# Kernel optimization log

Measured on AMD Instinct MI355X. Metric: run time of the kernel, lower is better.

The kernel has to match this reference:

```python
import jax, jax.numpy as jnp
import numpy as np

# Hexagonal 7-tap kernel mask on a 3x3 grid (axial coords): corners (0,2) and (2,0) unused.
_HEX = np.ones((3, 3), np.float32)
_HEX[0, 2] = 0.0
_HEX[2, 0] = 0.0
HEX_MASK = jnp.asarray(_HEX)
BN_EPS = 1e-5


def ico_pad(x):
    # x: [B,C,H,W] with H = 5 charts stacked. Cross-chart wrap pad along H
    # (neighbor-chart gather), zero pad along W (corner_mode='zeros').
    x = jnp.pad(x, ((0, 0), (0, 0), (1, 1), (0, 0)), mode='wrap')
    x = jnp.pad(x, ((0, 0), (0, 0), (0, 0), (1, 1)))
    return x


def ico_conv(x, w):
    # hex conv = masked 3x3 conv on icosahedrally padded charts
    return jax.lax.conv_general_dilated(
        ico_pad(x), w * HEX_MASK, window_strides=(1, 1), padding='VALID',
        dimension_numbers=('NCHW', 'OIHW', 'NCHW'))


def ico_upsample(x):
    # nearest-neighbor upsample to next subdivision (x2 per chart axis)
    return jnp.repeat(jnp.repeat(x, 2, axis=2), 2, axis=3)


def batchnorm(x, gamma, beta):
    # training-mode BatchNorm2d: stats over (B,H,W) per channel
    mean = x.mean(axis=(0, 2, 3), keepdims=True)
    var = x.var(axis=(0, 2, 3), keepdims=True)
    xhat = (x - mean) * jax.lax.rsqrt(var + BN_EPS)
    return xhat * gamma[:, None, None] + beta[:, None, None]


def setup_inputs() -> dict:
    key = jax.random.key(0)
    ks = jax.random.split(key, 10)
    B, Cin, Cout = 16, 64, 32
    H, W = 160, 64  # 5 charts of 32x64 (subdivision 5)
    x = jax.random.normal(ks[0], (B, Cin, H, W), dtype=jnp.float32)
    s0 = 1.0 / np.sqrt(Cin * 7)
    s1 = 1.0 / np.sqrt(Cout * 7)
    w00 = jax.random.normal(ks[1], (Cout, Cin, 3, 3), jnp.float32) * s0
    w01 = jax.random.normal(ks[2], (Cout, Cout, 3, 3), jnp.float32) * s1
    w10 = jax.random.normal(ks[3], (Cout, Cin, 3, 3), jnp.float32) * s0
    g00 = 1.0 + 0.1 * jax.random.normal(ks[4], (Cout,), jnp.float32)
    b00 = 0.1 * jax.random.normal(ks[5], (Cout,), jnp.float32)
    g01 = 1.0 + 0.1 * jax.random.normal(ks[6], (Cout,), jnp.float32)
    b01 = 0.1 * jax.random.normal(ks[7], (Cout,), jnp.float32)
    g10 = 1.0 + 0.1 * jax.random.normal(ks[8], (Cout,), jnp.float32)
    b10 = 0.1 * jax.random.normal(ks[9], (Cout,), jnp.float32)
    return {"x": x, "w00": w00, "w01": w01, "w10": w10,
            "g00": g00, "b00": b00, "g01": g01, "b01": b01,
            "g10": g10, "b10": b10}


def reference(x, w00, w01, w10, g00, b00, g01, b01, g10, b10):
    up = ico_upsample(x)  # [B,Cin,320,128]
    h = jax.nn.relu(batchnorm(ico_conv(up, w00), g00, b00))
    out0 = batchnorm(ico_conv(h, w01), g01, b01)
    out1 = batchnorm(ico_conv(up, w10), g10, b10)
    return jax.nn.relu(out0 + out1)
```

## Files before the change

kernel.cpp:

```cpp
#include <hip/hip_runtime.h>
#include <hip/hip_bf16.h>


#define CIN   64
#define COUT  32
#define HX    160
#define WX    64
#define HY    320
#define WY    128
#define NB    16
#define BN_EPS 1e-5f

typedef short s16x8 __attribute__((ext_vector_type(8)));
typedef float f32x4 __attribute__((ext_vector_type(4)));

__global__ __launch_bounds__(256) void prep_x(const float* __restrict__ x,
                                              __hip_bfloat16* __restrict__ xt)
{
    __shared__ float tile[64][65];
    const int n  = blockIdx.y;
    const int p0 = blockIdx.x * 64;
    const int t  = threadIdx.x;
#pragma unroll
    for (int e = 0; e < 16; ++e) {
        int k = e * 256 + t;
        int ci = k >> 6, p = k & 63;
        tile[ci][p] = x[(n * CIN + ci) * (HX * WX) + p0 + p];
    }
    __syncthreads();
#pragma unroll
    for (int e = 0; e < 16; ++e) {
        int k = e * 256 + t;
        int p = k >> 6, ci = k & 63;
        xt[((size_t)n * (HX * WX) + p0 + p) * 64 + ci] = __float2bfloat16(tile[ci][p]);
    }
}

__global__ __launch_bounds__(256) void prep_w(const float* __restrict__ w00,
                                              const float* __restrict__ w01,
                                              const float* __restrict__ w10,
                                              __hip_bfloat16* __restrict__ wAb,
                                              __hip_bfloat16* __restrict__ wBb)
{
    int t = blockIdx.x * 256 + threadIdx.x;
    if (t < 4096) {
        int cv = t >> 11, u = t & 2047;
        int co = u >> 6, ci = u & 63;
        const float* w = (cv ? w10 : w00) + (co * 64 + ci) * 9;
        float a = w[0], b = w[1], c = w[3], d = w[4], e5 = w[5], f = w[7], g = w[8];
        float v[16];
        v[0] = a;             v[1] = b;           v[2] = c;       v[3] = d + e5 + f + g;
        v[4] = a + b;         v[5] = c + d + f;   v[6] = e5 + g;  v[7] = 0.f;
        v[8] = a + c;         v[9] = b + d + e5;  v[10] = f + g;  v[11] = 0.f;
        v[12] = a + b + c + d; v[13] = e5;        v[14] = f;      v[15] = g;
#pragma unroll
        for (int s = 0; s < 16; ++s)
            wAb[(((size_t)cv * 16 + s) * 32 + co) * 64 + ci] = __float2bfloat16(v[s]);
    } else if (t < 5120) {
        int u = t - 4096;
        int co = u >> 5, ci = u & 31;
        const float* w = w01 + (co * 32 + ci) * 9;
        const int wi[7] = {0, 1, 3, 4, 5, 7, 8};
#pragma unroll
        for (int s = 0; s < 7; ++s)
            wBb[((size_t)s * 32 + co) * 32 + ci] = __float2bfloat16(w[wi[s]]);
    }
}

__global__ __launch_bounds__(256) void convA(
    const __hip_bfloat16* __restrict__ xt, const __hip_bfloat16* __restrict__ wAb,
    __hip_bfloat16* __restrict__ y0h, __hip_bfloat16* __restrict__ y1h,
    float* __restrict__ partialsA)
{
    __shared__ short lds[324 * 72];
    const int tb = blockIdx.x & 3, ta = blockIdx.x >> 2;
    const int nb = blockIdx.y, cv = blockIdx.z;
    const int t = threadIdx.x, wave = t >> 6, lane = t & 63;
    const int n = lane & 15, q = lane >> 4;
    const int a0 = ta * 16, b0 = tb * 16;

    for (int idx = t; idx < 2592; idx += 256) {
        int chunk = idx >> 3, sub = idx & 7;
        int rl = chunk / 18, cl = chunk - rl * 18;
        int grow = a0 - 1 + rl;
        if (grow < 0) grow += HX; else if (grow >= HX) grow -= HX;
        int gcol = b0 - 1 + cl;
        uint4 v = make_uint4(0u, 0u, 0u, 0u);
        if ((unsigned)gcol < (unsigned)WX)
            v = *(const uint4*)(xt + (((size_t)nb * HX + grow) * WX + gcol) * 64 + sub * 8);
        *(uint4*)(&lds[chunk * 72 + sub * 8]) = v;
    }
    __syncthreads();

    const int dr16[16] = {-1,-1, 0, 0,  -1, 0, 0, 0,   0, 0, 1, 0,   0, 0, 1, 1};
    const int dc16[16] = {-1, 0,-1, 0,   0, 0, 1, 0,  -1, 0, 0, 0,   0, 1, 0, 1};

    float st[2][4], sq2[2][4];
#pragma unroll
    for (int h = 0; h < 2; ++h)
#pragma unroll
        for (int r = 0; r < 4; ++r) { st[h][r] = 0.f; sq2[h][r] = 0.f; }

#pragma unroll
    for (int ph = 0; ph < 4; ++ph) {
        const int pa = ph >> 1, pb = ph & 1;
        s16x8 A[4][2][2];
#pragma unroll
        for (int ti = 0; ti < 4; ++ti)
#pragma unroll
            for (int kc = 0; kc < 2; ++kc)
#pragma unroll
                for (int h = 0; h < 2; ++h)
                    A[ti][kc][h] = *(const s16x8*)(wAb +
                        (((size_t)cv * 16 + ph * 4 + ti) * 32 + h * 16 + n) * 64 + kc * 32 + q * 8);
#pragma unroll
        for (int rr = 0; rr < 4; ++rr) {
            const int rl = wave * 4 + rr;
            s16x8 B[4][2];
#pragma unroll
            for (int ti = 0; ti < 4; ++ti) {
                const int off = ((rl + 1 + dr16[ph * 4 + ti]) * 18 + (n + 1 + dc16[ph * 4 + ti])) * 72;
#pragma unroll
                for (int kc = 0; kc < 2; ++kc)
                    B[ti][kc] = *(const s16x8*)(&lds[off + kc * 32 + q * 8]);
            }
            f32x4 acc[2];
            acc[0] = (f32x4){0.f, 0.f, 0.f, 0.f};
            acc[1] = (f32x4){0.f, 0.f, 0.f, 0.f};
#pragma unroll
            for (int ti = 0; ti < 4; ++ti)
#pragma unroll
                for (int kc = 0; kc < 2; ++kc)
#pragma unroll
                    for (int h = 0; h < 2; ++h)
                        acc[h] = __builtin_amdgcn_mfma_f32_16x16x32_bf16(
                            A[ti][kc][h], B[ti][kc], acc[h], 0, 0, 0);
            const int i = 2 * (a0 + rl) + pa;
            const int j = 2 * b0 + pb + 2 * n;
            if (cv == 0) {
                __hip_bfloat16* p = y0h + (((size_t)nb * HY + i) * WY + j) * 32;
#pragma unroll
                for (int h = 0; h < 2; ++h) {
                    __hip_bfloat162 lo = __float22bfloat162_rn(make_float2(acc[h][0], acc[h][1]));
                    __hip_bfloat162 hi = __float22bfloat162_rn(make_float2(acc[h][2], acc[h][3]));
                    __hip_bfloat162* pp = (__hip_bfloat162*)(p + h * 16 + q * 4);
                    pp[0] = lo; pp[1] = hi;
                }
            } else {
#pragma unroll
                for (int h = 0; h < 2; ++h)
#pragma unroll
                    for (int r = 0; r < 4; ++r) {
                        const int co = h * 16 + q * 4 + r;
                        y1h[(((size_t)nb * 32 + co) * HY + i) * WY + j] =
                            __float2bfloat16(acc[h][r]);
                    }
            }
#pragma unroll
            for (int h = 0; h < 2; ++h)
#pragma unroll
                for (int r = 0; r < 4; ++r) {
                    float v = acc[h][r];
                    st[h][r] += v; sq2[h][r] += v * v;
                }
        }
    }

    __syncthreads();
    float* scratch = (float*)lds;
#pragma unroll
    for (int h = 0; h < 2; ++h)
#pragma unroll
        for (int r = 0; r < 4; ++r) {
            float s = st[h][r], qv = sq2[h][r];
#pragma unroll
            for (int m = 1; m < 16; m <<= 1) {
                s  += __shfl_xor(s, m, 16);
                qv += __shfl_xor(qv, m, 16);
            }
            if (n == 0) {
                const int co = h * 16 + q * 4 + r;
                scratch[(wave * 32 + co) * 2]     = s;
                scratch[(wave * 32 + co) * 2 + 1] = qv;
            }
        }
    __syncthreads();
    if (t < 64) {
        const int co = t & 31, which = t >> 5;
        float s = scratch[(0 * 32 + co) * 2 + which] + scratch[(1 * 32 + co) * 2 + which]
                + scratch[(2 * 32 + co) * 2 + which] + scratch[(3 * 32 + co) * 2 + which];
        const int blk = blockIdx.y * 40 + blockIdx.x;
        partialsA[((size_t)cv * 640 + blk) * 64 + which * 32 + co] = s;
    }
}

__global__ __launch_bounds__(256) void reduce16(const float* __restrict__ src,
                                                float* __restrict__ dst)
{
    __shared__ float red[4][64];
    const int t = threadIdx.x, c = t & 63, seg = t >> 6;
    const float* s = src + (size_t)blockIdx.x * 16 * 64;
    float acc = 0.f;
#pragma unroll
    for (int r = 0; r < 4; ++r) acc += s[(seg + r * 4) * 64 + c];
    red[seg][c] = acc;
    __syncthreads();
    if (t < 64)
        dst[(size_t)blockIdx.x * 64 + t] = red[0][t] + red[1][t] + red[2][t] + red[3][t];
}

__global__ void params_h_kernel(const float* __restrict__ redA,
                                const float* __restrict__ g00,
                                const float* __restrict__ b00,
                                float* __restrict__ phs)
{
    __shared__ float tot[64];
    const int t = threadIdx.x;
    float s = 0.f;
    for (int b = 0; b < 40; ++b) s += redA[b * 64 + t];
    tot[t] = s;
    __syncthreads();
    if (t < 32) {
        const float nf = (float)(NB * HY * WY);
        float mean = tot[t] / nf;
        float var  = tot[32 + t] / nf - mean * mean;
        float sc = g00[t] * rsqrtf(var + BN_EPS);
        phs[t] = sc;
        phs[32 + t] = b00[t] - mean * sc;
    }
}

__global__ __launch_bounds__(256) void convB(
    const __hip_bfloat16* __restrict__ y0h, const __hip_bfloat16* __restrict__ wBb,
    const float* __restrict__ phs, __hip_bfloat16* __restrict__ y2h,
    float* __restrict__ partialsB)
{
    __shared__ short lds[612 * 40];
    const int tj = blockIdx.x & 3, ti = blockIdx.x >> 2;
    const int nb = blockIdx.y;
    const int t = threadIdx.x, wave = t >> 6, lane = t & 63;
    const int n = lane & 15, q = lane >> 4;
    const int i0 = ti * 16, j0 = tj * 32;

    const int cis = (t & 3) * 8;
    float sv[8], tv[8];
#pragma unroll
    for (int e = 0; e < 8; ++e) { sv[e] = phs[cis + e]; tv[e] = phs[32 + cis + e]; }

    for (int idx = t; idx < 2448; idx += 256) {
        int chunk = idx >> 2, sub = idx & 3;
        int rl = chunk / 34, cl = chunk - rl * 34;
        int grow = i0 - 1 + rl;
        if (grow < 0) grow += HY; else if (grow >= HY) grow -= HY;
        int gcol = j0 - 1 + cl;
        uint4 w = make_uint4(0u, 0u, 0u, 0u);
        if ((unsigned)gcol < (unsigned)WY) {
            uint4 v = *(const uint4*)(y0h + (((size_t)nb * HY + grow) * WY + gcol) * 32 + sub * 8);
            unsigned* vi = (unsigned*)&v;
            unsigned* wi = (unsigned*)&w;
#pragma unroll
            for (int k = 0; k < 4; ++k) {
                unsigned u = vi[k];
                float f0 = __uint_as_float(u << 16);
                float f1 = __uint_as_float(u & 0xffff0000u);
                f0 = fmaxf(fmaf(f0, sv[2 * k], tv[2 * k]), 0.f);
                f1 = fmaxf(fmaf(f1, sv[2 * k + 1], tv[2 * k + 1]), 0.f);
                union { __hip_bfloat162 b2; unsigned u32; } cvt;
                cvt.b2 = __float22bfloat162_rn(make_float2(f0, f1));
                wi[k] = cvt.u32;
            }
        }
        *(uint4*)(&lds[chunk * 40 + sub * 8]) = w;
    }
    __syncthreads();

    s16x8 A[7][2];
#pragma unroll
    for (int s = 0; s < 7; ++s)
#pragma unroll
        for (int h = 0; h < 2; ++h)
            A[s][h] = *(const s16x8*)(wBb + ((size_t)s * 32 + h * 16 + n) * 32 + q * 8);

    const int dr7[7] = {-1, -1, 0, 0, 0, 1, 1};
    const int dc7[7] = {-1,  0,-1, 0, 1, 0, 1};

    float st[2][4], sq2[2][4];
#pragma unroll
    for (int h = 0; h < 2; ++h)
#pragma unroll
        for (int r = 0; r < 4; ++r) { st[h][r] = 0.f; sq2[h][r] = 0.f; }

#pragma unroll
    for (int rr = 0; rr < 4; ++rr) {
        const int rl = wave * 4 + rr;
#pragma unroll
        for (int cg = 0; cg < 2; ++cg) {
            s16x8 B[7];
#pragma unroll
            for (int s = 0; s < 7; ++s)
                B[s] = *(const s16x8*)(&lds[((rl + 1 + dr7[s]) * 34 +
                                             (cg * 16 + n + 1 + dc7[s])) * 40 + q * 8]);
            f32x4 acc[2];
            acc[0] = (f32x4){0.f, 0.f, 0.f, 0.f};
            acc[1] = (f32x4){0.f, 0.f, 0.f, 0.f};
#pragma unroll
            for (int s = 0; s < 7; ++s)
#pragma unroll
                for (int h = 0; h < 2; ++h)
                    acc[h] = __builtin_amdgcn_mfma_f32_16x16x32_bf16(
                        A[s][h], B[s], acc[h], 0, 0, 0);
            const int i = i0 + rl;
            const int j = j0 + cg * 16 + n;
#pragma unroll
            for (int h = 0; h < 2; ++h)
#pragma unroll
                for (int r = 0; r < 4; ++r) {
                    const int co = h * 16 + q * 4 + r;
                    float v = acc[h][r];
                    y2h[(((size_t)nb * 32 + co) * HY + i) * WY + j] = __float2bfloat16(v);
                    st[h][r] += v; sq2[h][r] += v * v;
                }
        }
    }

    __syncthreads();
    float* scratch = (float*)lds;
#pragma unroll
    for (int h = 0; h < 2; ++h)
#pragma unroll
        for (int r = 0; r < 4; ++r) {
            float s = st[h][r], qv = sq2[h][r];
#pragma unroll
            for (int m = 1; m < 16; m <<= 1) {
                s  += __shfl_xor(s, m, 16);
                qv += __shfl_xor(qv, m, 16);
            }
            if (n == 0) {
                const int co = h * 16 + q * 4 + r;
                scratch[(wave * 32 + co) * 2]     = s;
                scratch[(wave * 32 + co) * 2 + 1] = qv;
            }
        }
    __syncthreads();
    if (t < 64) {
        const int co = t & 31, which = t >> 5;
        float s = scratch[(0 * 32 + co) * 2 + which] + scratch[(1 * 32 + co) * 2 + which]
                + scratch[(2 * 32 + co) * 2 + which] + scratch[(3 * 32 + co) * 2 + which];
        const int blk = blockIdx.y * 80 + blockIdx.x;
        partialsB[(size_t)blk * 64 + which * 32 + co] = s;
    }
}

__global__ void params_final_kernel(const float* __restrict__ redA,
                                    const float* __restrict__ redB,
                                    const float* __restrict__ g01,
                                    const float* __restrict__ b01,
                                    const float* __restrict__ g10,
                                    const float* __restrict__ b10,
                                    float* __restrict__ pf)
{
    __shared__ float tot1[64], tot2[64];
    const int t = threadIdx.x;
    float s1 = 0.f, s2 = 0.f;
    for (int b = 0; b < 40; ++b) s1 += redA[(40 + b) * 64 + t];
    for (int b = 0; b < 80; ++b) s2 += redB[b * 64 + t];
    tot1[t] = s1; tot2[t] = s2;
    __syncthreads();
    if (t < 32) {
        const float nf = (float)(NB * HY * WY);
        float m1 = tot1[t] / nf;
        float v1 = tot1[32 + t] / nf - m1 * m1;
        float sc1 = g10[t] * rsqrtf(v1 + BN_EPS);
        pf[t] = sc1;
        pf[32 + t] = b10[t] - m1 * sc1;
        float m2 = tot2[t] / nf;
        float v2 = tot2[32 + t] / nf - m2 * m2;
        float sc2 = g01[t] * rsqrtf(v2 + BN_EPS);
        pf[64 + t] = sc2;
        pf[96 + t] = b01[t] - m2 * sc2;
    }
}

__global__ __launch_bounds__(256) void final_kernel(
    const __hip_bfloat16* __restrict__ y1h, const __hip_bfloat16* __restrict__ y2h,
    const float* __restrict__ pf, float* __restrict__ out)
{
    const size_t e0 = ((size_t)blockIdx.x * 256 + threadIdx.x) * 8;
    const int c = (int)((e0 / (HY * WY)) & 31);
    const float s1 = pf[c], t1 = pf[32 + c];
    const float s2 = pf[64 + c], t2 = pf[96 + c];
    uint4 a = *(const uint4*)(y2h + e0);
    uint4 d = *(const uint4*)(y1h + e0);
    const unsigned* ai = (const unsigned*)&a;
    const unsigned* di = (const unsigned*)&d;
    float r[8];
#pragma unroll
    for (int k = 0; k < 4; ++k) {
        float a0 = __uint_as_float(ai[k] << 16);
        float a1 = __uint_as_float(ai[k] & 0xffff0000u);
        float d0 = __uint_as_float(di[k] << 16);
        float d1 = __uint_as_float(di[k] & 0xffff0000u);
        float r0 = fmaf(a0, s2, t2) + fmaf(d0, s1, t1);
        float r1 = fmaf(a1, s2, t2) + fmaf(d1, s1, t1);
        r[2 * k]     = r0 > 0.f ? r0 : 0.f;
        r[2 * k + 1] = r1 > 0.f ? r1 : 0.f;
    }
    float4* o = (float4*)(out + e0);
    o[0] = make_float4(r[0], r[1], r[2], r[3]);
    o[1] = make_float4(r[4], r[5], r[6], r[7]);
}

extern "C" void kernel_launch(void* const* d_in, const int* in_sizes, int n_in,
                              void* d_out, int out_size, void* d_ws, size_t ws_size,
                              hipStream_t stream)
{
    (void)in_sizes; (void)n_in; (void)out_size; (void)ws_size;
    const float* x   = (const float*)d_in[0];
    const float* w00 = (const float*)d_in[1];
    const float* w01 = (const float*)d_in[2];
    const float* w10 = (const float*)d_in[3];
    const float* g00 = (const float*)d_in[4];
    const float* b00 = (const float*)d_in[5];
    const float* g01 = (const float*)d_in[6];
    const float* b01 = (const float*)d_in[7];
    const float* g10 = (const float*)d_in[8];
    const float* b10 = (const float*)d_in[9];
    float* out = (float*)d_out;

    char* ws = (char*)d_ws;
    const size_t NPLANE = (size_t)NB * COUT * HY * WY;
    __hip_bfloat16* y1h  = (__hip_bfloat16*)ws;               ws += NPLANE * 2;
    __hip_bfloat16* y2h  = (__hip_bfloat16*)ws;               ws += NPLANE * 2;
    __hip_bfloat16* y0h  = (__hip_bfloat16*)ws;               ws += NPLANE * 2;
    __hip_bfloat16* xt   = (__hip_bfloat16*)ws;               ws += (size_t)NB * CIN * HX * WX * 2;
    __hip_bfloat16* wAb  = (__hip_bfloat16*)ws;               ws += 2 * 16 * 32 * 64 * 2;
    __hip_bfloat16* wBb  = (__hip_bfloat16*)ws;               ws += 7 * 32 * 32 * 2 + 256;
    float*          pA   = (float*)ws;                        ws += 2 * 640 * 64 * 4;
    float*          pB   = (float*)ws;                        ws += 1280 * 64 * 4;
    float*          redA = (float*)ws;                        ws += 80 * 64 * 4;
    float*          redB = (float*)ws;                        ws += 80 * 64 * 4;
    float*          phs  = (float*)ws;                        ws += 256;
    float*          pf   = (float*)ws;

    prep_x<<<dim3(160, 16), dim3(256), 0, stream>>>(x, xt);
    prep_w<<<dim3(20), dim3(256), 0, stream>>>(w00, w01, w10, wAb, wBb);
    convA<<<dim3(40, 16, 2), dim3(256), 0, stream>>>(xt, wAb, y0h, y1h, pA);
    reduce16<<<dim3(80), dim3(256), 0, stream>>>(pA, redA);
    params_h_kernel<<<dim3(1), dim3(64), 0, stream>>>(redA, g00, b00, phs);
    convB<<<dim3(80, 16), dim3(256), 0, stream>>>(y0h, wBb, phs, y2h, pB);
    reduce16<<<dim3(80), dim3(256), 0, stream>>>(pB, redB);
    params_final_kernel<<<dim3(1), dim3(64), 0, stream>>>(redA, redB, g01, b01, g10, b10, pf);
    final_kernel<<<dim3((int)(NPLANE / 8 / 256)), dim3(256), 0, stream>>>(y1h, y2h, pf, out);
}
```

Baseline: 268.5 us.

## Fuse both upsampled convs per block, store NHWC bf16, transpose in final pass

convA now computes both convolutions (w00 and w10) from a single staged input tile instead of one per grid z-slice, and drops the zero-padded phase taps from 16 to 14. y1 and y2 intermediates are stored channels-last as packed 4-wide bf16 stores instead of scattered 2-byte channel-planar writes. final_kernel transposes back to NCHW through LDS. Tiles are halved in height for more blocks, so there are more partial-stat blocks to reduce. The trade-off is that weights are now loaded from global memory inside the MFMA loop rather than hoisted, and the final pass gains an LDS transpose.

```diff
diff --git a/kernel.cpp b/kernel.cpp
--- a/kernel.cpp
+++ b/kernel.cpp
@@ -14,6 +14,13 @@
 typedef short s16x8 __attribute__((ext_vector_type(8)));
 typedef float f32x4 __attribute__((ext_vector_type(4)));
 
+__device__ inline void store_bf16x4(__hip_bfloat16* p, f32x4 v) {
+    union { unsigned long long u; __hip_bfloat162 h[2]; } pk;
+    pk.h[0] = __float22bfloat162_rn(make_float2(v[0], v[1]));
+    pk.h[1] = __float22bfloat162_rn(make_float2(v[2], v[3]));
+    *(unsigned long long*)p = pk.u;
+}
+
 __global__ __launch_bounds__(256) void prep_x(const float* __restrict__ x,
                                               __hip_bfloat16* __restrict__ xt)
 {
@@ -48,14 +55,14 @@
         int co = u >> 6, ci = u & 63;
         const float* w = (cv ? w10 : w00) + (co * 64 + ci) * 9;
         float a = w[0], b = w[1], c = w[3], d = w[4], e5 = w[5], f = w[7], g = w[8];
-        float v[16];
-        v[0] = a;             v[1] = b;           v[2] = c;       v[3] = d + e5 + f + g;
-        v[4] = a + b;         v[5] = c + d + f;   v[6] = e5 + g;  v[7] = 0.f;
-        v[8] = a + c;         v[9] = b + d + e5;  v[10] = f + g;  v[11] = 0.f;
-        v[12] = a + b + c + d; v[13] = e5;        v[14] = f;      v[15] = g;
-#pragma unroll
-        for (int s = 0; s < 16; ++s)
-            wAb[(((size_t)cv * 16 + s) * 32 + co) * 64 + ci] = __float2bfloat16(v[s]);
+        float v[14];
+        v[0] = a;              v[1] = b;          v[2] = c;      v[3] = d + e5 + f + g;
+        v[4] = a + b;          v[5] = c + d + f;  v[6] = e5 + g;
+        v[7] = a + c;          v[8] = b + d + e5; v[9] = f + g;
+        v[10] = a + b + c + d; v[11] = e5;        v[12] = f;     v[13] = g;
+#pragma unroll
+        for (int s = 0; s < 14; ++s)
+            wAb[(((size_t)cv * 14 + s) * 32 + co) * 64 + ci] = __float2bfloat16(v[s]);
     } else if (t < 5120) {
         int u = t - 4096;
         int co = u >> 5, ci = u & 31;
@@ -72,14 +79,14 @@
     __hip_bfloat16* __restrict__ y0h, __hip_bfloat16* __restrict__ y1h,
     float* __restrict__ partialsA)
 {
-    __shared__ short lds[324 * 72];
+    __shared__ short lds[180 * 72];
     const int tb = blockIdx.x & 3, ta = blockIdx.x >> 2;
-    const int nb = blockIdx.y, cv = blockIdx.z;
+    const int nb = blockIdx.y;
     const int t = threadIdx.x, wave = t >> 6, lane = t & 63;
     const int n = lane & 15, q = lane >> 4;
-    const int a0 = ta * 16, b0 = tb * 16;
-
-    for (int idx = t; idx < 2592; idx += 256) {
+    const int a0 = ta * 8, b0 = tb * 16;
+
+    for (int idx = t; idx < 1440; idx += 256) {
         int chunk = idx >> 3, sub = idx & 7;
         int rl = chunk / 18, cl = chunk - rl * 18;
         int grow = a0 - 1 + rl;
@@ -92,105 +99,96 @@
     }
     __syncthreads();
 
-    const int dr16[16] = {-1,-1, 0, 0,  -1, 0, 0, 0,   0, 0, 1, 0,   0, 0, 1, 1};
-    const int dc16[16] = {-1, 0,-1, 0,   0, 0, 1, 0,  -1, 0, 0, 0,   0, 1, 0, 1};
-
-    float st[2][4], sq2[2][4];
-#pragma unroll
-    for (int h = 0; h < 2; ++h)
-#pragma unroll
-        for (int r = 0; r < 4; ++r) { st[h][r] = 0.f; sq2[h][r] = 0.f; }
+    const int off14[5] = {0, 4, 7, 10, 14};
+    const int dr14[14] = {-1,-1, 0, 0,  -1, 0, 0,   0, 0, 1,   0, 0, 1, 1};
+    const int dc14[14] = {-1, 0,-1, 0,   0, 0, 1,  -1, 0, 0,   0, 1, 0, 1};
+
+    f32x4 st[2][2], sq[2][2];
+#pragma unroll
+    for (int cv = 0; cv < 2; ++cv)
+#pragma unroll
+        for (int h = 0; h < 2; ++h) {
+            st[cv][h] = (f32x4){0.f, 0.f, 0.f, 0.f};
+            sq[cv][h] = (f32x4){0.f, 0.f, 0.f, 0.f};
+        }
 
 #pragma unroll
     for (int ph = 0; ph < 4; ++ph) {
         const int pa = ph >> 1, pb = ph & 1;
-        s16x8 A[4][2][2];
-#pragma unroll
-        for (int ti = 0; ti < 4; ++ti)
-#pragma unroll
-            for (int kc = 0; kc < 2; ++kc)
-#pragma unroll
-                for (int h = 0; h < 2; ++h)
-                    A[ti][kc][h] = *(const s16x8*)(wAb +
-                        (((size_t)cv * 16 + ph * 4 + ti) * 32 + h * 16 + n) * 64 + kc * 32 + q * 8);
-#pragma unroll
-        for (int rr = 0; rr < 4; ++rr) {
-            const int rl = wave * 4 + rr;
+        const int s0 = off14[ph], s1 = off14[ph + 1];
+#pragma unroll
+        for (int rr = 0; rr < 2; ++rr) {
+            const int rl = wave * 2 + rr;
             s16x8 B[4][2];
 #pragma unroll
-            for (int ti = 0; ti < 4; ++ti) {
-                const int off = ((rl + 1 + dr16[ph * 4 + ti]) * 18 + (n + 1 + dc16[ph * 4 + ti])) * 72;
-#pragma unroll
-                for (int kc = 0; kc < 2; ++kc)
-                    B[ti][kc] = *(const s16x8*)(&lds[off + kc * 32 + q * 8]);
-            }
-            f32x4 acc[2];
-            acc[0] = (f32x4){0.f, 0.f, 0.f, 0.f};
-            acc[1] = (f32x4){0.f, 0.f, 0.f, 0.f};
-#pragma unroll
-            for (int ti = 0; ti < 4; ++ti)
-#pragma unroll
-                for (int kc = 0; kc < 2; ++kc)
-#pragma unroll
-                    for (int h = 0; h < 2; ++h)
-                        acc[h] = __builtin_amdgcn_mfma_f32_16x16x32_bf16(
-                            A[ti][kc][h], B[ti][kc], acc[h], 0, 0, 0);
+            for (int s = s0; s < s1; ++s) {
+                const int o = ((rl + 1 + dr14[s]) * 18 + (n + 1 + dc14[s])) * 72;
+                B[s - s0][0] = *(const s16x8*)(&lds[o + q * 8]);
+                B[s - s0][1] = *(const s16x8*)(&lds[o + 32 + q * 8]);
+            }
+            f32x4 acc[2][2];
+#pragma unroll
+            for (int cv = 0; cv < 2; ++cv)
+#pragma unroll
+                for (int h = 0; h < 2; ++h) acc[cv][h] = (f32x4){0.f, 0.f, 0.f, 0.f};
+#pragma unroll
+            for (int cv = 0; cv < 2; ++cv)
+#pragma unroll
+                for (int s = s0; s < s1; ++s)
+#pragma unroll
+                    for (int kc = 0; kc < 2; ++kc)
+#pragma unroll
+                        for (int h = 0; h < 2; ++h) {
+                            s16x8 A = *(const s16x8*)(wAb +
+                                (((size_t)cv * 14 + s) * 32 + h * 16 + n) * 64 + kc * 32 + q * 8);
+                            acc[cv][h] = __builtin_amdgcn_mfma_f32_16x16x32_bf16(
+                                A, B[s - s0][kc], acc[cv][h], 0, 0, 0);
+                        }
             const int i = 2 * (a0 + rl) + pa;
             const int j = 2 * b0 + pb + 2 * n;
-            if (cv == 0) {
-                __hip_bfloat16* p = y0h + (((size_t)nb * HY + i) * WY + j) * 32;
+            const size_t obase = ((((size_t)nb * HY + i) * WY + j) * 32) + q * 4;
+#pragma unroll
+            for (int cv = 0; cv < 2; ++cv) {
+                __hip_bfloat16* yp = cv ? y1h : y0h;
 #pragma unroll
                 for (int h = 0; h < 2; ++h) {
-                    __hip_bfloat162 lo = __float22bfloat162_rn(make_float2(acc[h][0], acc[h][1]));
-                    __hip_bfloat162 hi = __float22bfloat162_rn(make_float2(acc[h][2], acc[h][3]));
-                    __hip_bfloat162* pp = (__hip_bfloat162*)(p + h * 16 + q * 4);
-                    pp[0] = lo; pp[1] = hi;
+                    store_bf16x4(yp + obase + h * 16, acc[cv][h]);
+                    st[cv][h] += acc[cv][h];
+                    sq[cv][h] += acc[cv][h] * acc[cv][h];
                 }
-            } else {
-#pragma unroll
-                for (int h = 0; h < 2; ++h)
-#pragma unroll
-                    for (int r = 0; r < 4; ++r) {
-                        const int co = h * 16 + q * 4 + r;
-                        y1h[(((size_t)nb * 32 + co) * HY + i) * WY + j] =
-                            __float2bfloat16(acc[h][r]);
-                    }
-            }
-#pragma unroll
-            for (int h = 0; h < 2; ++h)
-#pragma unroll
-                for (int r = 0; r < 4; ++r) {
-                    float v = acc[h][r];
-                    st[h][r] += v; sq2[h][r] += v * v;
+            }
+        }
+    }
+
+    __syncthreads();
+    float* scr = (float*)lds;
+#pragma unroll
+    for (int cv = 0; cv < 2; ++cv)
+#pragma unroll
+        for (int h = 0; h < 2; ++h)
+#pragma unroll
+            for (int r = 0; r < 4; ++r) {
+                float s = st[cv][h][r], qv = sq[cv][h][r];
+#pragma unroll
+                for (int m = 1; m < 16; m <<= 1) {
+                    s  += __shfl_xor(s, m, 16);
+                    qv += __shfl_xor(qv, m, 16);
                 }
-        }
-    }
-
-    __syncthreads();
-    float* scratch = (float*)lds;
-#pragma unroll
-    for (int h = 0; h < 2; ++h)
-#pragma unroll
-        for (int r = 0; r < 4; ++r) {
-            float s = st[h][r], qv = sq2[h][r];
-#pragma unroll
-            for (int m = 1; m < 16; m <<= 1) {
-                s  += __shfl_xor(s, m, 16);
-                qv += __shfl_xor(qv, m, 16);
-            }
-            if (n == 0) {
-                const int co = h * 16 + q * 4 + r;
-                scratch[(wave * 32 + co) * 2]     = s;
-                scratch[(wave * 32 + co) * 2 + 1] = qv;
-            }
-        }
-    __syncthreads();
-    if (t < 64) {
-        const int co = t & 31, which = t >> 5;
-        float s = scratch[(0 * 32 + co) * 2 + which] + scratch[(1 * 32 + co) * 2 + which]
-                + scratch[(2 * 32 + co) * 2 + which] + scratch[(3 * 32 + co) * 2 + which];
-        const int blk = blockIdx.y * 40 + blockIdx.x;
-        partialsA[((size_t)cv * 640 + blk) * 64 + which * 32 + co] = s;
+                if (n == 0) {
+                    const int co = h * 16 + q * 4 + r;
+                    scr[(((wave * 2 + cv) * 32) + co) * 2]     = s;
+                    scr[(((wave * 2 + cv) * 32) + co) * 2 + 1] = qv;
+                }
+            }
+    __syncthreads();
+    if (t < 128) {
+        const int cv = t >> 6, which = (t >> 5) & 1, co = t & 31;
+        float s = 0.f;
+#pragma unroll
+        for (int w = 0; w < 4; ++w)
+            s += scr[(((w * 2 + cv) * 32) + co) * 2 + which];
+        const int blk = nb * 80 + blockIdx.x;
+        partialsA[((size_t)cv * 1280 + blk) * 64 + which * 32 + co] = s;
     }
 }
 
@@ -217,7 +215,7 @@
     __shared__ float tot[64];
     const int t = threadIdx.x;
     float s = 0.f;
-    for (int b = 0; b < 40; ++b) s += redA[b * 64 + t];
+    for (int b = 0; b < 80; ++b) s += redA[b * 64 + t];
     tot[t] = s;
     __syncthreads();
     if (t < 32) {
@@ -235,19 +233,19 @@
     const float* __restrict__ phs, __hip_bfloat16* __restrict__ y2h,
     float* __restrict__ partialsB)
 {
-    __shared__ short lds[612 * 40];
+    __shared__ short lds[340 * 40];
     const int tj = blockIdx.x & 3, ti = blockIdx.x >> 2;
     const int nb = blockIdx.y;
     const int t = threadIdx.x, wave = t >> 6, lane = t & 63;
     const int n = lane & 15, q = lane >> 4;
-    const int i0 = ti * 16, j0 = tj * 32;
+    const int i0 = ti * 8, j0 = tj * 32;
 
     const int cis = (t & 3) * 8;
     float sv[8], tv[8];
 #pragma unroll
     for (int e = 0; e < 8; ++e) { sv[e] = phs[cis + e]; tv[e] = phs[32 + cis + e]; }
 
-    for (int idx = t; idx < 2448; idx += 256) {
+    for (int idx = t; idx < 1360; idx += 256) {
         int chunk = idx >> 2, sub = idx & 3;
         int rl = chunk / 34, cl = chunk - rl * 34;
         int grow = i0 - 1 + rl;
@@ -284,15 +282,13 @@
     const int dr7[7] = {-1, -1, 0, 0, 0, 1, 1};
     const int dc7[7] = {-1,  0,-1, 0, 1, 0, 1};
 
-    float st[2][4], sq2[2][4];
-#pragma unroll
-    for (int h = 0; h < 2; ++h)
-#pragma unroll
-        for (int r = 0; r < 4; ++r) { st[h][r] = 0.f; sq2[h][r] = 0.f; }
-
-#pragma unroll
-    for (int rr = 0; rr < 4; ++rr) {
-        const int rl = wave * 4 + rr;
+    f32x4 st[2], sq[2];
+    st[0] = st[1] = (f32x4){0.f, 0.f, 0.f, 0.f};
+    sq[0] = sq[1] = (f32x4){0.f, 0.f, 0.f, 0.f};
+
+#pragma unroll
+    for (int rr = 0; rr < 2; ++rr) {
+        const int rl = wave * 2 + rr;
 #pragma unroll
         for (int cg = 0; cg < 2; ++cg) {
             s16x8 B[7];
@@ -311,25 +307,23 @@
                         A[s][h], B[s], acc[h], 0, 0, 0);
             const int i = i0 + rl;
             const int j = j0 + cg * 16 + n;
-#pragma unroll
-            for (int h = 0; h < 2; ++h)
-#pragma unroll
-                for (int r = 0; r < 4; ++r) {
-                    const int co = h * 16 + q * 4 + r;
-                    float v = acc[h][r];
-                    y2h[(((size_t)nb * 32 + co) * HY + i) * WY + j] = __float2bfloat16(v);
-                    st[h][r] += v; sq2[h][r] += v * v;
-                }
-        }
-    }
-
-    __syncthreads();
-    float* scratch = (float*)lds;
+            const size_t obase = ((((size_t)nb * HY + i) * WY + j) * 32) + q * 4;
+#pragma unroll
+            for (int h = 0; h < 2; ++h) {
+                store_bf16x4(y2h + obase + h * 16, acc[h]);
+                st[h] += acc[h];
+                sq[h] += acc[h] * acc[h];
+            }
+        }
+    }
+
+    __syncthreads();
+    float* scr = (float*)lds;
 #pragma unroll
     for (int h = 0; h < 2; ++h)
 #pragma unroll
         for (int r = 0; r < 4; ++r) {
-            float s = st[h][r], qv = sq2[h][r];
+            float s = st[h][r], qv = sq[h][r];
 #pragma unroll
             for (int m = 1; m < 16; m <<= 1) {
                 s  += __shfl_xor(s, m, 16);
@@ -337,16 +331,17 @@
             }
             if (n == 0) {
                 const int co = h * 16 + q * 4 + r;
-                scratch[(wave * 32 + co) * 2]     = s;
-                scratch[(wave * 32 + co) * 2 + 1] = qv;
+                scr[(wave * 32 + co) * 2]     = s;
+                scr[(wave * 32 + co) * 2 + 1] = qv;
             }
         }
     __syncthreads();
     if (t < 64) {
         const int co = t & 31, which = t >> 5;
-        float s = scratch[(0 * 32 + co) * 2 + which] + scratch[(1 * 32 + co) * 2 + which]
-                + scratch[(2 * 32 + co) * 2 + which] + scratch[(3 * 32 + co) * 2 + which];
-        const int blk = blockIdx.y * 80 + blockIdx.x;
+        float s = 0.f;
+#pragma unroll
+        for (int w = 0; w < 4; ++w) s += scr[(w * 32 + co) * 2 + which];
+        const int blk = nb * 160 + blockIdx.x;
         partialsB[(size_t)blk * 64 + which * 32 + co] = s;
     }
 }
@@ -362,8 +357,8 @@
     __shared__ float tot1[64], tot2[64];
     const int t = threadIdx.x;
     float s1 = 0.f, s2 = 0.f;
-    for (int b = 0; b < 40; ++b) s1 += redA[(40 + b) * 64 + t];
-    for (int b = 0; b < 80; ++b) s2 += redB[b * 64 + t];
+    for (int b = 0; b < 80; ++b)  s1 += redA[(80 + b) * 64 + t];
+    for (int b = 0; b < 160; ++b) s2 += redB[b * 64 + t];
     tot1[t] = s1; tot2[t] = s2;
     __syncthreads();
     if (t < 32) {
@@ -385,29 +380,52 @@
     const __hip_bfloat16* __restrict__ y1h, const __hip_bfloat16* __restrict__ y2h,
     const float* __restrict__ pf, float* __restrict__ out)
 {
-    const size_t e0 = ((size_t)blockIdx.x * 256 + threadIdx.x) * 8;
-    const int c = (int)((e0 / (HY * WY)) & 31);
-    const float s1 = pf[c], t1 = pf[32 + c];
-    const float s2 = pf[64 + c], t2 = pf[96 + c];
-    uint4 a = *(const uint4*)(y2h + e0);
-    uint4 d = *(const uint4*)(y1h + e0);
-    const unsigned* ai = (const unsigned*)&a;
-    const unsigned* di = (const unsigned*)&d;
-    float r[8];
-#pragma unroll
-    for (int k = 0; k < 4; ++k) {
-        float a0 = __uint_as_float(ai[k] << 16);
-        float a1 = __uint_as_float(ai[k] & 0xffff0000u);
-        float d0 = __uint_as_float(di[k] << 16);
-        float d1 = __uint_as_float(di[k] & 0xffff0000u);
-        float r0 = fmaf(a0, s2, t2) + fmaf(d0, s1, t1);
-        float r1 = fmaf(a1, s2, t2) + fmaf(d1, s1, t1);
-        r[2 * k]     = r0 > 0.f ? r0 : 0.f;
-        r[2 * k + 1] = r1 > 0.f ? r1 : 0.f;
-    }
-    float4* o = (float4*)(out + e0);
-    o[0] = make_float4(r[0], r[1], r[2], r[3]);
-    o[1] = make_float4(r[4], r[5], r[6], r[7]);
+    __shared__ float ldsf[32 * 132];
+    const int nb = blockIdx.y;
+    const int i0 = blockIdx.x * 2;
+    const int t = threadIdx.x;
+    const int c8 = (t & 3) * 8;
+
+    float P1s[8], P1t[8], P2s[8], P2t[8];
+#pragma unroll
+    for (int e = 0; e < 8; ++e) {
+        P1s[e] = pf[c8 + e];      P1t[e] = pf[32 + c8 + e];
+        P2s[e] = pf[64 + c8 + e]; P2t[e] = pf[96 + c8 + e];
+    }
+
+    for (int row = 0; row < 2; ++row) {
+        const int i = i0 + row;
+        const size_t base = (((size_t)nb * HY + i) * WY) * 32;
+        if (row) __syncthreads();
+#pragma unroll
+        for (int rep = 0; rep < 2; ++rep) {
+            const int idx = rep * 256 + t;
+            const int j = idx >> 2;
+            uint4 a = *(const uint4*)(y2h + base + (size_t)j * 32 + c8);
+            uint4 d = *(const uint4*)(y1h + base + (size_t)j * 32 + c8);
+            const unsigned* ai = (const unsigned*)&a;
+            const unsigned* di = (const unsigned*)&d;
+#pragma unroll
+            for (int k = 0; k < 4; ++k) {
+                float a0 = __uint_as_float(ai[k] << 16);
+                float a1 = __uint_as_float(ai[k] & 0xffff0000u);
+                float d0 = __uint_as_float(di[k] << 16);
+                float d1 = __uint_as_float(di[k] & 0xffff0000u);
+                float r0 = fmaf(a0, P2s[2 * k], P2t[2 * k]) + fmaf(d0, P1s[2 * k], P1t[2 * k]);
+                float r1 = fmaf(a1, P2s[2 * k + 1], P2t[2 * k + 1]) + fmaf(d1, P1s[2 * k + 1], P1t[2 * k + 1]);
+                ldsf[(c8 + 2 * k) * 132 + j]     = r0 > 0.f ? r0 : 0.f;
+                ldsf[(c8 + 2 * k + 1) * 132 + j] = r1 > 0.f ? r1 : 0.f;
+            }
+        }
+        __syncthreads();
+#pragma unroll
+        for (int rep = 0; rep < 4; ++rep) {
+            const int idx = rep * 256 + t;
+            const int co = idx >> 5, jg = (idx & 31) * 4;
+            float4 v = *(float4*)(&ldsf[co * 132 + jg]);
+            *(float4*)(out + (((size_t)nb * 32 + co) * HY + i) * WY + jg) = v;
+        }
+    }
 }
 
 extern "C" void kernel_launch(void* const* d_in, const int* in_sizes, int n_in,
@@ -433,22 +451,22 @@
     __hip_bfloat16* y2h  = (__hip_bfloat16*)ws;               ws += NPLANE * 2;
     __hip_bfloat16* y0h  = (__hip_bfloat16*)ws;               ws += NPLANE * 2;
     __hip_bfloat16* xt   = (__hip_bfloat16*)ws;               ws += (size_t)NB * CIN * HX * WX * 2;
-    __hip_bfloat16* wAb  = (__hip_bfloat16*)ws;               ws += 2 * 16 * 32 * 64 * 2;
-    __hip_bfloat16* wBb  = (__hip_bfloat16*)ws;               ws += 7 * 32 * 32 * 2 + 256;
-    float*          pA   = (float*)ws;                        ws += 2 * 640 * 64 * 4;
-    float*          pB   = (float*)ws;                        ws += 1280 * 64 * 4;
-    float*          redA = (float*)ws;                        ws += 80 * 64 * 4;
-    float*          redB = (float*)ws;                        ws += 80 * 64 * 4;
+    __hip_bfloat16* wAb  = (__hip_bfloat16*)ws;               ws += 2 * 14 * 32 * 64 * 2;
+    __hip_bfloat16* wBb  = (__hip_bfloat16*)ws;               ws += 7 * 32 * 32 * 2;
+    float*          pA   = (float*)ws;                        ws += 2 * 1280 * 64 * 4;
+    float*          pB   = (float*)ws;                        ws += 2560 * 64 * 4;
+    float*          redA = (float*)ws;                        ws += 160 * 64 * 4;
+    float*          redB = (float*)ws;                        ws += 160 * 64 * 4;
     float*          phs  = (float*)ws;                        ws += 256;
     float*          pf   = (float*)ws;
 
     prep_x<<<dim3(160, 16), dim3(256), 0, stream>>>(x, xt);
     prep_w<<<dim3(20), dim3(256), 0, stream>>>(w00, w01, w10, wAb, wBb);
-    convA<<<dim3(40, 16, 2), dim3(256), 0, stream>>>(xt, wAb, y0h, y1h, pA);
-    reduce16<<<dim3(80), dim3(256), 0, stream>>>(pA, redA);
+    convA<<<dim3(80, 16), dim3(256), 0, stream>>>(xt, wAb, y0h, y1h, pA);
+    reduce16<<<dim3(160), dim3(256), 0, stream>>>(pA, redA);
     params_h_kernel<<<dim3(1), dim3(64), 0, stream>>>(redA, g00, b00, phs);
-    convB<<<dim3(80, 16), dim3(256), 0, stream>>>(y0h, wBb, phs, y2h, pB);
-    reduce16<<<dim3(80), dim3(256), 0, stream>>>(pB, redB);
+    convB<<<dim3(160, 16), dim3(256), 0, stream>>>(y0h, wBb, phs, y2h, pB);
+    reduce16<<<dim3(160), dim3(256), 0, stream>>>(pB, redB);
     params_final_kernel<<<dim3(1), dim3(64), 0, stream>>>(redA, redB, g01, b01, g10, b10, pf);
-    final_kernel<<<dim3((int)(NPLANE / 8 / 256)), dim3(256), 0, stream>>>(y1h, y2h, pf, out);
-}
+    final_kernel<<<dim3(160, 16), dim3(256), 0, stream>>>(y1h, y2h, pf, out);
+}
```

Result: slower. 351.8 us (+31.0%).
